# Optimization experiments

Hardware: AMD Instinct MI355X
Metric: run time of the kernel (lower is better)

The kernel has to match this reference:

```python
import jax, jax.numpy as jnp
import numpy as np
import math

EMBED_DIM = 1024
NUM_HEADS = 16
HEAD_DIM = EMBED_DIM // NUM_HEADS
ACT_BITS = 8
WGT_BITS = 8


def fake_quant(x, n_bits):
    # Per-tensor symmetric fake quantization with straight-through estimator.
    qmax = 2.0 ** (n_bits - 1) - 1.0  # 127 for 8 bits
    scale = jnp.maximum(jnp.max(jnp.abs(x)) / qmax, 1e-8)
    q = jnp.clip(jnp.round(x / scale), -qmax - 1.0, qmax) * scale
    return x + jax.lax.stop_gradient(q - x)


def setup_inputs() -> dict:
    key = jax.random.key(0)
    ks = jax.random.split(key, 7)
    S, B, D = 2048, 2, EMBED_DIM
    return {
        "query": jax.random.normal(ks[0], (S, B, D), dtype=jnp.float32),
        "key": jax.random.normal(ks[1], (S, B, D), dtype=jnp.float32),
        "value": jax.random.normal(ks[2], (S, B, D), dtype=jnp.float32),
        "Wi": jax.random.normal(ks[3], (3 * D, D), dtype=jnp.float32) * (1.0 / math.sqrt(D)),
        "bi": jax.random.normal(ks[4], (3 * D,), dtype=jnp.float32) * 0.01,
        "Wo": jax.random.normal(ks[5], (D, D), dtype=jnp.float32) * (1.0 / math.sqrt(D)),
        "bo": jax.random.normal(ks[6], (D,), dtype=jnp.float32) * 0.01,
    }


def reference(query, key, value, Wi, bi, Wo, bo):
    D, H, hd = EMBED_DIM, NUM_HEADS, HEAD_DIM
    len_q, batch, _ = query.shape
    len_k = key.shape[0]

    Wi_q = fake_quant(Wi, WGT_BITS)
    Wo_q = fake_quant(Wo, WGT_BITS)

    # in-projections (full 3D projection per input, then chunk, as in source)
    Xq = fake_quant(query @ Wi_q.T + bi, ACT_BITS)
    Xk = fake_quant(key @ Wi_q.T + bi, ACT_BITS)
    Xv = fake_quant(value @ Wi_q.T + bi, ACT_BITS)
    Q = Xq[..., :D]
    K = Xk[..., D:2 * D]
    V = Xv[..., 2 * D:]

    # [len, B, D] -> [B*H, len, hd]
    q = Q.reshape(len_q, batch * H, hd).transpose(1, 0, 2)
    k = K.reshape(len_k, batch * H, hd).transpose(1, 0, 2)
    v = V.reshape(len_k, batch * H, hd).transpose(1, 0, 2)

    q = fake_quant(q / math.sqrt(hd), ACT_BITS)
    attn = jnp.einsum('bqd,bkd->bqk', q, k)  # note: attn/softmax fake-quants in source are no-ops (result discarded)
    attn = jax.nn.softmax(attn, axis=-1)
    heads = fake_quant(jnp.einsum('bqk,bkd->bqd', attn, v), ACT_BITS)

    # [B*H, len_q, hd] -> [len_q*B, D]
    heads_reshape = heads.transpose(1, 0, 2).reshape(len_q * batch, D)
    y = (heads_reshape @ Wo_q.T + bo).reshape(len_q, batch, D)
    return fake_quant(y, ACT_BITS)
```

## Files before the change

kernel.cpp:

```cpp
#include <hip/hip_runtime.h>
#include <math.h>


typedef _Float16 f16;
typedef _Float16 half8 __attribute__((ext_vector_type(8)));
typedef _Float16 half4 __attribute__((ext_vector_type(4)));
typedef _Float16 half2v __attribute__((ext_vector_type(2)));
typedef __fp16 fp16x2 __attribute__((ext_vector_type(2)));
typedef float floatx4 __attribute__((ext_vector_type(4)));
typedef int int4v __attribute__((ext_vector_type(4)));

#define QMAX 127.0f

#define SLOT_WI 0
#define SLOT_WO 1
#define SLOT_XQ 2
#define SLOT_XK 3
#define SLOT_XV 4
#define SLOT_HD 5
#define SLOT_Y  6
#define SLOT_Q  7
#define SLOT_A  8

__device__ __forceinline__ float slot_scale(const unsigned* slots, int slot, float premul) {
  if (slot < 0) return 1.0f;
  return fmaxf(__uint_as_float(slots[slot]) * premul / QMAX, 1e-8f);
}

__device__ __forceinline__ float slot_scaleA(const unsigned* slots) {
  return fmaxf(__uint_as_float(slots[SLOT_A]) / 16256.0f, 1e-8f);
}

__device__ __forceinline__ void gl2lds16(const void* gsrc, void* ldst) {
  __builtin_amdgcn_global_load_lds((__attribute__((address_space(1))) void*)gsrc,
                                   (__attribute__((address_space(3))) void*)ldst, 16, 0, 0);
}

__device__ __forceinline__ half2v pack2(float a, float b) {
  fp16x2 r = __builtin_amdgcn_cvt_pkrtz(a, b);
  return __builtin_bit_cast(half2v, r);
}

__global__ __launch_bounds__(64) void init_slots_k(unsigned* slots) {
  if (threadIdx.x < 16) slots[threadIdx.x] = 0u;
}

__global__ __launch_bounds__(256) void absmax3_k(const float* __restrict__ Wi,
                                                 const float* __restrict__ Wo,
                                                 const float* __restrict__ q,
                                                 const float* __restrict__ k,
                                                 const float* __restrict__ v,
                                                 unsigned* __restrict__ slots) {
  __shared__ float red[256];
  int tid = threadIdx.x;
  int bid = blockIdx.x;
  const float4* x4;
  int n4, i0, stride, slot;
  if (bid < 768) {
    x4 = (const float4*)Wi; n4 = 786432; i0 = bid * 256 + tid;
    stride = 768 * 256; slot = SLOT_WI;
  } else if (bid < 1024) {
    x4 = (const float4*)Wo; n4 = 262144; i0 = (bid - 768) * 256 + tid;
    stride = 256 * 256; slot = SLOT_WO;
  } else {
    int r = bid - 1024;
    int t = r >> 9;
    x4 = (const float4*)(t == 0 ? q : (t == 1 ? k : v));
    n4 = 1048576; i0 = (r & 511) * 256 + tid;
    stride = 512 * 256; slot = SLOT_A;
  }
  float lmax = 0.f;
  for (int i = i0; i < n4; i += stride) {
    float4 vv = x4[i];
    lmax = fmaxf(lmax, fmaxf(fmaxf(fabsf(vv.x), fabsf(vv.y)), fmaxf(fabsf(vv.z), fabsf(vv.w))));
  }
  red[tid] = lmax; __syncthreads();
  for (int sh = 128; sh > 0; sh >>= 1) {
    if (tid < sh) red[tid] = fmaxf(red[tid], red[tid + sh]);
    __syncthreads();
  }
  if (tid == 0) atomicMax(&slots[slot], __float_as_uint(red[0]));
}

__global__ __launch_bounds__(256) void quantw_k(const float* __restrict__ Wi,
                                                const float* __restrict__ Wo,
                                                char* __restrict__ Wi8,
                                                char* __restrict__ Wo8,
                                                const unsigned* __restrict__ slots) {
  int tid = threadIdx.x;
  if (blockIdx.x < 768) {
    float s = slot_scale(slots, SLOT_WI, 1.0f);
    const float4* in4 = (const float4*)Wi;
    for (int i = blockIdx.x * 256 + tid; i < 786432; i += 768 * 256) {
      float4 v = in4[i];
      char4 o;
      o.x = (signed char)(int)fminf(fmaxf(rintf(v.x / s), -128.0f), 127.0f);
      o.y = (signed char)(int)fminf(fmaxf(rintf(v.y / s), -128.0f), 127.0f);
      o.z = (signed char)(int)fminf(fmaxf(rintf(v.z / s), -128.0f), 127.0f);
      o.w = (signed char)(int)fminf(fmaxf(rintf(v.w / s), -128.0f), 127.0f);
      *(char4*)(Wi8 + (size_t)i * 4) = o;
    }
  } else {
    float s = slot_scale(slots, SLOT_WO, 1.0f);
    const float4* in4 = (const float4*)Wo;
    for (int i = (blockIdx.x - 768) * 256 + tid; i < 262144; i += 256 * 256) {
      float4 v = in4[i];
      char4 o;
      o.x = (signed char)(int)fminf(fmaxf(rintf(v.x / s), -128.0f), 127.0f);
      o.y = (signed char)(int)fminf(fmaxf(rintf(v.y / s), -128.0f), 127.0f);
      o.z = (signed char)(int)fminf(fmaxf(rintf(v.z / s), -128.0f), 127.0f);
      o.w = (signed char)(int)fminf(fmaxf(rintf(v.w / s), -128.0f), 127.0f);
      *(char4*)(Wo8 + (size_t)i * 4) = o;
    }
  }
}

__global__ __launch_bounds__(256) void digitize_k(const float* __restrict__ q,
                                                  const float* __restrict__ k,
                                                  const float* __restrict__ v,
                                                  char* __restrict__ A1,
                                                  char* __restrict__ A2,
                                                  const unsigned* __restrict__ slots) {
  float inv = 1.0f / slot_scaleA(slots);
  char4* o1 = (char4*)A1;
  char4* o2 = (char4*)A2;
  for (int i = blockIdx.x * 256 + threadIdx.x; i < 3145728; i += gridDim.x * 256) {
    int t = i >> 20;
    const float4* src = (const float4*)(t == 0 ? q : (t == 1 ? k : v));
    float4 x = src[i & 1048575];
    float xs[4] = {x.x, x.y, x.z, x.w};
    signed char c1s[4], c2s[4];
#pragma unroll
    for (int u = 0; u < 4; ++u) {
      float qv = fminf(fmaxf(rintf(xs[u] * inv), -16256.0f), 16256.0f);
      float c1 = rintf(qv * 0.0078125f);
      c1s[u] = (signed char)(int)c1;
      c2s[u] = (signed char)(int)(qv - 128.0f * c1);
    }
    o1[i] = make_char4(c1s[0], c1s[1], c1s[2], c1s[3]);
    o2[i] = make_char4(c2s[0], c2s[1], c2s[2], c2s[3]);
  }
}

__global__ __launch_bounds__(256) void quantf_k(const float* __restrict__ in, float* __restrict__ out,
                                                int n4, unsigned* __restrict__ slots,
                                                int sSlot, float premul) {
  float s = slot_scale(slots, sSlot, premul);
  const float4* in4 = (const float4*)in;
  float4* out4 = (float4*)out;
  for (int i = blockIdx.x * 256 + threadIdx.x; i < n4; i += gridDim.x * 256) {
    float4 v = in4[i];
    float xs[4] = {v.x, v.y, v.z, v.w};
#pragma unroll
    for (int u = 0; u < 4; ++u) {
      float r = rintf((xs[u] * premul) / s);
      r = fminf(fmaxf(r, -128.0f), 127.0f);
      xs[u] = r * s;
    }
    out4[i] = make_float4(xs[0], xs[1], xs[2], xs[3]);
  }
}

__global__ __launch_bounds__(256) void quanti_k(const float* __restrict__ in, f16* __restrict__ out,
                                                int n4, unsigned* __restrict__ slots,
                                                int sSlot, int outAbsSlot) {
  __shared__ float red[256];
  float s = slot_scale(slots, sSlot, 1.0f);
  float lmax = 0.f;
  const float4* in4 = (const float4*)in;
  for (int i = blockIdx.x * 256 + threadIdx.x; i < n4; i += gridDim.x * 256) {
    float4 v = in4[i];
    float xs[4] = {v.x, v.y, v.z, v.w};
    half4 o;
#pragma unroll
    for (int u = 0; u < 4; ++u) {
      float r = rintf(xs[u] / s);
      r = fminf(fmaxf(r, -128.0f), 127.0f);
      o[u] = (f16)r;
      lmax = fmaxf(lmax, fabsf(r));
    }
    *(half4*)(out + (size_t)i * 4) = o;
  }
  if (outAbsSlot >= 0) {
    int tid = threadIdx.x;
    red[tid] = lmax; __syncthreads();
    for (int sh = 128; sh > 0; sh >>= 1) {
      if (tid < sh) red[tid] = fmaxf(red[tid], red[tid + sh]);
      __syncthreads();
    }
    if (tid == 0) atomicMax(&slots[outAbsSlot], __float_as_uint(red[0] * s));
  }
}

__global__ __launch_bounds__(256) void quant8_k(const float* __restrict__ in, char* __restrict__ out,
                                                int n4, const unsigned* __restrict__ slots,
                                                int sSlot) {
  float s = slot_scale(slots, sSlot, 1.0f);
  const float4* in4 = (const float4*)in;
  for (int i = blockIdx.x * 256 + threadIdx.x; i < n4; i += gridDim.x * 256) {
    float4 v = in4[i];
    char4 o;
    o.x = (signed char)(int)fminf(fmaxf(rintf(v.x / s), -128.0f), 127.0f);
    o.y = (signed char)(int)fminf(fmaxf(rintf(v.y / s), -128.0f), 127.0f);
    o.z = (signed char)(int)fminf(fmaxf(rintf(v.z / s), -128.0f), 127.0f);
    o.w = (signed char)(int)fminf(fmaxf(rintf(v.w / s), -128.0f), 127.0f);
    *(char4*)(out + (size_t)i * 4) = o;
  }
}

__global__ __launch_bounds__(256) void quantv_t_k(const float* __restrict__ Xv,
                                                  f16* __restrict__ Vt,
                                                  const unsigned* __restrict__ slots) {
  __shared__ f16 T[64][68];
  int tid = threadIdx.x;
  int bh = blockIdx.y, b = bh >> 4, h = bh & 15;
  int k0 = blockIdx.x * 64;
  float s = slot_scale(slots, SLOT_XV, 1.0f);
#pragma unroll
  for (int it = 0; it < 4; ++it) {
    int idx = tid + it * 256;
    int row = idx >> 4, dseg = idx & 15;
    float4 v = *(const float4*)(Xv + ((size_t)(k0 + row) * 2 + b) * 1024 + h * 64 + dseg * 4);
    float xs[4] = {v.x, v.y, v.z, v.w};
    half4 o;
#pragma unroll
    for (int u = 0; u < 4; ++u) {
      float r = rintf(xs[u] / s);
      o[u] = (f16)fminf(fmaxf(r, -128.0f), 127.0f);
    }
    *(half4*)&T[row][dseg * 4] = o;
  }
  __syncthreads();
#pragma unroll
  for (int it = 0; it < 2; ++it) {
    int sdx = tid + it * 256;
    int d = sdx >> 3, j8 = sdx & 7;
    half8 o;
#pragma unroll
    for (int l = 0; l < 8; ++l) {
      int pos = j8 * 8 + l;
      int tp = pos >> 5, pq = (pos & 31) >> 3, jj = pos & 7;
      int k = tp * 32 + pq * 4 + ((jj < 4) ? jj : jj + 12);
      o[l] = T[k][d];
    }
    *(half8*)(Vt + ((size_t)bh * 64 + d) * 2048 + k0 + j8 * 8) = o;
  }
}

__global__ __launch_bounds__(512, 4) void gemm_qkv_i8_k(const char* __restrict__ A1,
                                                        const char* __restrict__ A2,
                                                        const char* __restrict__ B8,
                                                        const float* __restrict__ bias,
                                                        float* __restrict__ Xout,
                                                        unsigned* __restrict__ slots) {
  __shared__ char As1[2][8192];
  __shared__ char As2[2][8192];
  __shared__ char Bs8[2][8192];
  __shared__ float red[512];

  const int K = 1024;
  int tid = threadIdx.x;
  int lane = tid & 63, w = tid >> 6;
  int wm = w >> 1, wn = w & 1;
  int quad = lane >> 4, l15 = lane & 15;
  int t = blockIdx.y >> 5;
  int m0 = (blockIdx.y & 31) * 128;
  int n0 = blockIdx.x * 128;
  size_t aoff = (size_t)t * 4194304;

  int srow = lane >> 2;
  int sgr = (lane & 3) * 16;

  const char* a1p = A1 + aoff;
  const char* a2p = A2 + aoff;

  int4v acc1[2][4], acc2[2][4];
#pragma unroll
  for (int i = 0; i < 2; ++i)
#pragma unroll
    for (int j = 0; j < 4; ++j) {
      acc1[i][j] = (int4v){0, 0, 0, 0};
      acc2[i][j] = (int4v){0, 0, 0, 0};
    }

  auto stage = [&](int buf, int kk) __attribute__((always_inline)) {
    int r0 = w * 16;
    int row = r0 + srow;
    gl2lds16(a1p + (size_t)(m0 + row) * K + kk + sgr, &As1[buf][r0 * 64]);
    gl2lds16(a2p + (size_t)(m0 + row) * K + kk + sgr, &As2[buf][r0 * 64]);
    gl2lds16(B8 + (size_t)(n0 + row) * K + kk + sgr, &Bs8[buf][r0 * 64]);
  };

  auto compute = [&](int buf) __attribute__((always_inline)) {
    int4v bf[4];
#pragma unroll
    for (int j = 0; j < 4; ++j)
      bf[j] = *(const int4v*)&Bs8[buf][(wn * 64 + j * 16 + l15) * 64 + quad * 16];
    int4v a1f[2];
#pragma unroll
    for (int i = 0; i < 2; ++i)
      a1f[i] = *(const int4v*)&As1[buf][(wm * 32 + i * 16 + l15) * 64 + quad * 16];
#pragma unroll
    for (int i = 0; i < 2; ++i)
#pragma unroll
      for (int j = 0; j < 4; ++j)
        acc1[i][j] = __builtin_amdgcn_mfma_i32_16x16x64_i8(a1f[i], bf[j], acc1[i][j], 0, 0, 0);
    int4v a2f[2];
#pragma unroll
    for (int i = 0; i < 2; ++i)
      a2f[i] = *(const int4v*)&As2[buf][(wm * 32 + i * 16 + l15) * 64 + quad * 16];
#pragma unroll
    for (int i = 0; i < 2; ++i)
#pragma unroll
      for (int j = 0; j < 4; ++j)
        acc2[i][j] = __builtin_amdgcn_mfma_i32_16x16x64_i8(a2f[i], bf[j], acc2[i][j], 0, 0, 0);
  };

  stage(0, 0);
  __syncthreads();
  for (int kt = 0; kt < 7; ++kt) {
    stage(1, (2 * kt + 1) * 64);
    compute(0);
    __syncthreads();
    stage(0, (2 * kt + 2) * 64);
    compute(1);
    __syncthreads();
  }
  stage(1, 960);
  compute(0);
  __syncthreads();
  compute(1);

  float sc = slot_scaleA(slots) * slot_scale(slots, SLOT_WI, 1.0f);
  int colLo = t * 1024;
  float* outT = Xout + aoff;
  float lmax = 0.f;
#pragma unroll
  for (int i = 0; i < 2; ++i) {
#pragma unroll
    for (int j = 0; j < 4; ++j) {
      int gn = n0 + wn * 64 + j * 16 + l15;
      float bv = bias[gn];
      bool wr = (gn >= colLo && gn < colLo + 1024);
#pragma unroll
      for (int r = 0; r < 4; ++r) {
        int gm = m0 + wm * 32 + i * 16 + quad * 4 + r;
        float vv = fmaf((float)acc1[i][j][r], 128.0f, (float)acc2[i][j][r]) * sc + bv;
        lmax = fmaxf(lmax, fabsf(vv));
        if (wr) outT[(size_t)gm * 1024 + (gn - colLo)] = vv;
      }
    }
  }
  red[tid] = lmax; __syncthreads();
  for (int sh = 256; sh > 0; sh >>= 1) {
    if (tid < sh) red[tid] = fmaxf(red[tid], red[tid + sh]);
    __syncthreads();
  }
  if (tid == 0) atomicMax(&slots[SLOT_XQ + t], __float_as_uint(red[0]));
}

__global__ __launch_bounds__(256) void gemm_i8out_k(const char* __restrict__ A8,
                                                    const char* __restrict__ B8,
                                                    const float* __restrict__ bias,
                                                    float* __restrict__ out,
                                                    unsigned* __restrict__ slots) {
  __shared__ char As8[2][8192];
  __shared__ char Bs8[2][8192];
  __shared__ float red[256];

  const int K = 1024;
  int tid = threadIdx.x;
  int lane = tid & 63, w = tid >> 6;
  int wm = w >> 1, wn = w & 1;
  int quad = lane >> 4, l15 = lane & 15;
  int m0 = blockIdx.y * 128, n0 = blockIdx.x * 128;

  int srow = lane >> 2;
  int sgr = (lane & 3) * 16;

  int4v acc[4][4];
#pragma unroll
  for (int i = 0; i < 4; ++i)
#pragma unroll
    for (int j = 0; j < 4; ++j) acc[i][j] = (int4v){0, 0, 0, 0};

  auto stage = [&](int buf, int kk) __attribute__((always_inline)) {
#pragma unroll
    for (int u = 0; u < 2; ++u) {
      int r0 = (w * 2 + u) * 16;
      int row = r0 + srow;
      gl2lds16(A8 + (size_t)(m0 + row) * K + kk + sgr, &As8[buf][r0 * 64]);
      gl2lds16(B8 + (size_t)(n0 + row) * K + kk + sgr, &Bs8[buf][r0 * 64]);
    }
  };

  auto compute = [&](int buf) __attribute__((always_inline)) {
    int4v af[4], bf[4];
#pragma unroll
    for (int i = 0; i < 4; ++i)
      af[i] = *(const int4v*)&As8[buf][(wm * 64 + i * 16 + l15) * 64 + quad * 16];
#pragma unroll
    for (int j = 0; j < 4; ++j)
      bf[j] = *(const int4v*)&Bs8[buf][(wn * 64 + j * 16 + l15) * 64 + quad * 16];
#pragma unroll
    for (int i = 0; i < 4; ++i)
#pragma unroll
      for (int j = 0; j < 4; ++j)
        acc[i][j] = __builtin_amdgcn_mfma_i32_16x16x64_i8(af[i], bf[j], acc[i][j], 0, 0, 0);
  };

  stage(0, 0);
  __syncthreads();
  for (int kt = 0; kt < 7; ++kt) {
    stage(1, (2 * kt + 1) * 64);
    compute(0);
    __syncthreads();
    stage(0, (2 * kt + 2) * 64);
    compute(1);
    __syncthreads();
  }
  stage(1, 960);
  compute(0);
  __syncthreads();
  compute(1);

  float sc = slot_scale(slots, SLOT_HD, 1.0f) * slot_scale(slots, SLOT_WO, 1.0f);
  float lmax = 0.f;
#pragma unroll
  for (int i = 0; i < 4; ++i) {
#pragma unroll
    for (int j = 0; j < 4; ++j) {
      int gn = n0 + wn * 64 + j * 16 + l15;
      float bv = bias[gn];
#pragma unroll
      for (int r = 0; r < 4; ++r) {
        int gm = m0 + wm * 64 + i * 16 + quad * 4 + r;
        float v = (float)acc[i][j][r] * sc + bv;
        lmax = fmaxf(lmax, fabsf(v));
        out[(size_t)gm * 1024 + gn] = v;
      }
    }
  }
  red[tid] = lmax; __syncthreads();
  for (int sh = 128; sh > 0; sh >>= 1) {
    if (tid < sh) red[tid] = fmaxf(red[tid], red[tid + sh]);
    __syncthreads();
  }
  if (tid == 0) atomicMax(&slots[SLOT_Y], __float_as_uint(red[0]));
}

__global__ __launch_bounds__(256) void attn_k(const f16* __restrict__ Qc,
                                              const f16* __restrict__ Kh,
                                              const f16* __restrict__ Vt,
                                              float* __restrict__ heads,
                                              unsigned* __restrict__ slots) {
  __shared__ f16 Ks[64 * 64];
  __shared__ f16 Vs[64][72];
  __shared__ float lred[4][2][16];
  __shared__ float red[256];

  int tid = threadIdx.x;
  int lane = tid & 63, w = tid >> 6;
  int quad = lane >> 4, l15 = lane & 15;
  int bh = blockIdx.y, b = bh >> 4, h = bh & 15;
  int q0 = blockIdx.x * 128;

  float s1 = slot_scale(slots, SLOT_XQ, 1.0f);
  float sq = slot_scale(slots, SLOT_Q, 0.125f);
  float sk = slot_scale(slots, SLOT_XK, 1.0f);
  float sv = slot_scale(slots, SLOT_XV, 1.0f);
  float cS = sq * sk * 1.44269504088896340736f;
  const float FOFF = 12.0f;

  half8 qf[2][2];
#pragma unroll
  for (int s = 0; s < 2; ++s) {
    const f16* qrow = Qc + ((size_t)(q0 + w * 32 + s * 16 + l15) * 2 + b) * 1024 + h * 64;
    half8 qr0 = *(const half8*)(qrow + quad * 8);
    half8 qr1 = *(const half8*)(qrow + 32 + quad * 8);
#pragma unroll
    for (int u = 0; u < 8; ++u) {
      float x0 = ((float)qr0[u] * s1) * 0.125f;
      float x1 = ((float)qr1[u] * s1) * 0.125f;
      qf[s][0][u] = (f16)fminf(fmaxf(rintf(x0 / sq), -128.0f), 127.0f);
      qf[s][1][u] = (f16)fminf(fmaxf(rintf(x1 / sq), -128.0f), 127.0f);
    }
  }

  int ksrow = lane >> 3;
  int ksp = lane & 7;
  int vr0 = tid >> 3, vs0 = (tid & 7) * 8;

  floatx4 oacc[2][4];
#pragma unroll
  for (int s = 0; s < 2; ++s)
#pragma unroll
    for (int d = 0; d < 4; ++d) oacc[s][d] = (floatx4){0.f, 0.f, 0.f, 0.f};
  float lsum[2] = {0.f, 0.f};

  const f16* vbase = Vt + (size_t)bh * 131072;

  for (int kt = 0; kt < 2048; kt += 64) {
    __syncthreads();
#pragma unroll
    for (int t = 0; t < 2; ++t) {
      int r0 = (w * 2 + t) * 8;
      int row = r0 + ksrow;
      int g = ksp ^ (row & 7);
      gl2lds16(Kh + ((size_t)(kt + row) * 2 + b) * 1024 + h * 64 + g * 8, &Ks[r0 * 64]);
    }
    half8 va = *(const half8*)(vbase + (size_t)vr0 * 2048 + kt + vs0);
    half8 vb = *(const half8*)(vbase + (size_t)(vr0 + 32) * 2048 + kt + vs0);
    *(half8*)&Vs[vr0][vs0] = va;
    *(half8*)&Vs[vr0 + 32][vs0] = vb;
    __syncthreads();

    half8 aph[2][2], apl[2][2];
#pragma unroll
    for (int t = 0; t < 4; ++t) {
      int row = t * 16 + l15;
      int g1 = quad ^ (row & 7);
      half8 kf0 = *(half8*)&Ks[row * 64 + g1 * 8];
      half8 kf1 = *(half8*)&Ks[row * 64 + (g1 ^ 4) * 8];
      int tp = t >> 1, hi = (t & 1) * 4;
#pragma unroll
      for (int s = 0; s < 2; ++s) {
        floatx4 sacc = (floatx4){0.f, 0.f, 0.f, 0.f};
        sacc = __builtin_amdgcn_mfma_f32_16x16x32_f16(kf0, qf[s][0], sacc, 0, 0, 0);
        sacc = __builtin_amdgcn_mfma_f32_16x16x32_f16(kf1, qf[s][1], sacc, 0, 0, 0);
        float p0 = __builtin_amdgcn_exp2f(fmaf(sacc[0], cS, -FOFF));
        float p1 = __builtin_amdgcn_exp2f(fmaf(sacc[1], cS, -FOFF));
        float p2 = __builtin_amdgcn_exp2f(fmaf(sacc[2], cS, -FOFF));
        float p3 = __builtin_amdgcn_exp2f(fmaf(sacc[3], cS, -FOFF));
        lsum[s] += (p0 + p1) + (p2 + p3);
        half2v h01 = pack2(p0, p1);
        half2v h23 = pack2(p2, p3);
        half2v l01 = pack2(p0 - (float)h01[0], p1 - (float)h01[1]);
        half2v l23 = pack2(p2 - (float)h23[0], p3 - (float)h23[1]);
        aph[s][tp][hi + 0] = h01[0]; aph[s][tp][hi + 1] = h01[1];
        aph[s][tp][hi + 2] = h23[0]; aph[s][tp][hi + 3] = h23[1];
        apl[s][tp][hi + 0] = l01[0]; apl[s][tp][hi + 1] = l01[1];
        apl[s][tp][hi + 2] = l23[0]; apl[s][tp][hi + 3] = l23[1];
      }
    }

#pragma unroll
    for (int d = 0; d < 4; ++d) {
      const f16* vsrow = &Vs[d * 16 + l15][0];
      half8 b0 = *(const half8*)(vsrow + quad * 8);
      half8 b1 = *(const half8*)(vsrow + 32 + quad * 8);
#pragma unroll
      for (int s = 0; s < 2; ++s) {
        oacc[s][d] = __builtin_amdgcn_mfma_f32_16x16x32_f16(aph[s][0], b0, oacc[s][d], 0, 0, 0);
        oacc[s][d] = __builtin_amdgcn_mfma_f32_16x16x32_f16(apl[s][0], b0, oacc[s][d], 0, 0, 0);
        oacc[s][d] = __builtin_amdgcn_mfma_f32_16x16x32_f16(aph[s][1], b1, oacc[s][d], 0, 0, 0);
        oacc[s][d] = __builtin_amdgcn_mfma_f32_16x16x32_f16(apl[s][1], b1, oacc[s][d], 0, 0, 0);
      }
    }
  }

#pragma unroll
  for (int s = 0; s < 2; ++s) {
    float l = lsum[s];
    l += __shfl_xor(l, 16);
    l += __shfl_xor(l, 32);
    lred[w][s][l15] = l;
  }
  float linv[2][4];
#pragma unroll
  for (int s = 0; s < 2; ++s)
#pragma unroll
    for (int r = 0; r < 4; ++r) linv[s][r] = sv / lred[w][s][quad * 4 + r];

  float lmax = 0.f;
#pragma unroll
  for (int s = 0; s < 2; ++s)
#pragma unroll
    for (int d = 0; d < 4; ++d)
#pragma unroll
      for (int r = 0; r < 4; ++r) {
        float hv = oacc[s][d][r] * linv[s][r];
        heads[((size_t)(q0 + w * 32 + s * 16 + quad * 4 + r) * 2 + b) * 1024 +
              h * 64 + d * 16 + l15] = hv;
        lmax = fmaxf(lmax, fabsf(hv));
      }
  red[tid] = lmax; __syncthreads();
  for (int sh = 128; sh > 0; sh >>= 1) {
    if (tid < sh) red[tid] = fmaxf(red[tid], red[tid + sh]);
    __syncthreads();
  }
  if (tid == 0) atomicMax(&slots[SLOT_HD], __float_as_uint(red[0]));
}

extern "C" void kernel_launch(void* const* d_in, const int* in_sizes, int n_in,
                              void* d_out, int out_size, void* d_ws, size_t ws_size,
                              hipStream_t stream) {
  (void)in_sizes; (void)n_in; (void)out_size; (void)ws_size;
  const float* query = (const float*)d_in[0];
  const float* key   = (const float*)d_in[1];
  const float* value = (const float*)d_in[2];
  const float* Wi    = (const float*)d_in[3];
  const float* bi    = (const float*)d_in[4];
  const float* Wo    = (const float*)d_in[5];
  const float* bo    = (const float*)d_in[6];
  float* out = (float*)d_out;

  char* p = (char*)d_ws;
  unsigned* slots = (unsigned*)p;            p += 1024;
  char* Wi8 = p;                             p += 3072 * 1024;
  char* Wo8 = p;                             p += 1024 * 1024;
  char* A1  = p;                             p += 12288 * 1024;
  char* A2  = p;                             p += 12288 * 1024;
  float* Hd = (float*)A1;
  f16* Kint = (f16*)(A2 + 4194304);
  float* Xq = (float*)p;                     p += 4096 * 1024 * 4;
  float* Y  = Xq;
  float* Xk = (float*)p;                     p += 4096 * 1024 * 4;
  f16* Qc   = (f16*)Xk;
  float* Xv = (float*)p;                     p += 4096 * 1024 * 4;
  char* Hint8 = (char*)Xv + 4096 * 1024 * 2;
  f16* Vt   = (f16*)p;                       p += 4096 * 1024 * 2;

  init_slots_k<<<1, 64, 0, stream>>>(slots);
  absmax3_k<<<2560, 256, 0, stream>>>(Wi, Wo, query, key, value, slots);
  quantw_k<<<1024, 256, 0, stream>>>(Wi, Wo, Wi8, Wo8, slots);
  digitize_k<<<2048, 256, 0, stream>>>(query, key, value, A1, A2, slots);

  dim3 gq(24, 96);
  gemm_qkv_i8_k<<<gq, 512, 0, stream>>>(A1, A2, Wi8, bi, Xq, slots);

  quanti_k<<<1024, 256, 0, stream>>>(Xk, Kint, 1048576, slots, SLOT_XK, -1);
  quanti_k<<<1024, 256, 0, stream>>>(Xq, Qc, 1048576, slots, SLOT_XQ, SLOT_Q);

  dim3 gvt(32, 32);
  quantv_t_k<<<gvt, 256, 0, stream>>>(Xv, Vt, slots);

  dim3 ga(16, 32);
  attn_k<<<ga, 256, 0, stream>>>(Qc, Kint, Vt, Hd, slots);

  quant8_k<<<1024, 256, 0, stream>>>(Hd, Hint8, 1048576, slots, SLOT_HD);

  dim3 g2(8, 32);
  gemm_i8out_k<<<g2, 256, 0, stream>>>(Hint8, Wo8, bo, Y, slots);

  quantf_k<<<1024, 256, 0, stream>>>(Y, out, 1048576, slots, SLOT_Y, 1.0f);
}
```

Before: 372.2 us.

## Pre-swizzle int8 GEMM operands into MFMA tile layout and widen output GEMM blocks

```diff
diff --git a/kernel.cpp b/kernel.cpp
--- a/kernel.cpp
+++ b/kernel.cpp
@@ -39,6 +39,11 @@
 __device__ __forceinline__ half2v pack2(float a, float b) {
   fp16x2 r = __builtin_amdgcn_cvt_pkrtz(a, b);
   return __builtin_bit_cast(half2v, r);
+}
+
+__device__ __forceinline__ size_t swz(int m, int k) {
+  return ((size_t)(m >> 4) << 14) + (size_t)(((k >> 6) << 10) +
+         (((k >> 4) & 3) << 8) + ((m & 15) << 4) + (k & 15));
 }
 
 __global__ __launch_bounds__(64) void init_slots_k(unsigned* slots) {
@@ -93,24 +98,26 @@
     const float4* in4 = (const float4*)Wi;
     for (int i = blockIdx.x * 256 + tid; i < 786432; i += 768 * 256) {
       float4 v = in4[i];
+      int n = i >> 8, kk = (i & 255) * 4;
       char4 o;
       o.x = (signed char)(int)fminf(fmaxf(rintf(v.x / s), -128.0f), 127.0f);
       o.y = (signed char)(int)fminf(fmaxf(rintf(v.y / s), -128.0f), 127.0f);
       o.z = (signed char)(int)fminf(fmaxf(rintf(v.z / s), -128.0f), 127.0f);
       o.w = (signed char)(int)fminf(fmaxf(rintf(v.w / s), -128.0f), 127.0f);
-      *(char4*)(Wi8 + (size_t)i * 4) = o;
+      *(char4*)(Wi8 + swz(n, kk)) = o;
     }
   } else {
     float s = slot_scale(slots, SLOT_WO, 1.0f);
     const float4* in4 = (const float4*)Wo;
     for (int i = (blockIdx.x - 768) * 256 + tid; i < 262144; i += 256 * 256) {
       float4 v = in4[i];
+      int n = i >> 8, kk = (i & 255) * 4;
       char4 o;
       o.x = (signed char)(int)fminf(fmaxf(rintf(v.x / s), -128.0f), 127.0f);
       o.y = (signed char)(int)fminf(fmaxf(rintf(v.y / s), -128.0f), 127.0f);
       o.z = (signed char)(int)fminf(fmaxf(rintf(v.z / s), -128.0f), 127.0f);
       o.w = (signed char)(int)fminf(fmaxf(rintf(v.w / s), -128.0f), 127.0f);
-      *(char4*)(Wo8 + (size_t)i * 4) = o;
+      *(char4*)(Wo8 + swz(n, kk)) = o;
     }
   }
 }
@@ -122,12 +129,12 @@
                                                   char* __restrict__ A2,
                                                   const unsigned* __restrict__ slots) {
   float inv = 1.0f / slot_scaleA(slots);
-  char4* o1 = (char4*)A1;
-  char4* o2 = (char4*)A2;
   for (int i = blockIdx.x * 256 + threadIdx.x; i < 3145728; i += gridDim.x * 256) {
     int t = i >> 20;
+    int g = i & 1048575;
     const float4* src = (const float4*)(t == 0 ? q : (t == 1 ? k : v));
-    float4 x = src[i & 1048575];
+    float4 x = src[g];
+    int m = g >> 8, kk = (g & 255) * 4;
     float xs[4] = {x.x, x.y, x.z, x.w};
     signed char c1s[4], c2s[4];
 #pragma unroll
@@ -137,8 +144,9 @@
       c1s[u] = (signed char)(int)c1;
       c2s[u] = (signed char)(int)(qv - 128.0f * c1);
     }
-    o1[i] = make_char4(c1s[0], c1s[1], c1s[2], c1s[3]);
-    o2[i] = make_char4(c2s[0], c2s[1], c2s[2], c2s[3]);
+    size_t off = (size_t)t * 4194304 + swz(m, kk);
+    *(char4*)(A1 + off) = make_char4(c1s[0], c1s[1], c1s[2], c1s[3]);
+    *(char4*)(A2 + off) = make_char4(c2s[0], c2s[1], c2s[2], c2s[3]);
   }
 }
 
@@ -199,12 +207,13 @@
   const float4* in4 = (const float4*)in;
   for (int i = blockIdx.x * 256 + threadIdx.x; i < n4; i += gridDim.x * 256) {
     float4 v = in4[i];
+    int m = i >> 8, kk = (i & 255) * 4;
     char4 o;
     o.x = (signed char)(int)fminf(fmaxf(rintf(v.x / s), -128.0f), 127.0f);
     o.y = (signed char)(int)fminf(fmaxf(rintf(v.y / s), -128.0f), 127.0f);
     o.z = (signed char)(int)fminf(fmaxf(rintf(v.z / s), -128.0f), 127.0f);
     o.w = (signed char)(int)fminf(fmaxf(rintf(v.w / s), -128.0f), 127.0f);
-    *(char4*)(out + (size_t)i * 4) = o;
+    *(char4*)(out + swz(m, kk)) = o;
   }
 }
 
@@ -247,18 +256,17 @@
   }
 }
 
-__global__ __launch_bounds__(512, 4) void gemm_qkv_i8_k(const char* __restrict__ A1,
-                                                        const char* __restrict__ A2,
-                                                        const char* __restrict__ B8,
-                                                        const float* __restrict__ bias,
-                                                        float* __restrict__ Xout,
-                                                        unsigned* __restrict__ slots) {
+__global__ __launch_bounds__(512) void gemm_qkv_i8_k(const char* __restrict__ A1,
+                                                     const char* __restrict__ A2,
+                                                     const char* __restrict__ B8,
+                                                     const float* __restrict__ bias,
+                                                     float* __restrict__ Xout,
+                                                     unsigned* __restrict__ slots) {
   __shared__ char As1[2][8192];
   __shared__ char As2[2][8192];
   __shared__ char Bs8[2][8192];
   __shared__ float red[512];
 
-  const int K = 1024;
   int tid = threadIdx.x;
   int lane = tid & 63, w = tid >> 6;
   int wm = w >> 1, wn = w & 1;
@@ -268,9 +276,6 @@
   int n0 = blockIdx.x * 128;
   size_t aoff = (size_t)t * 4194304;
 
-  int srow = lane >> 2;
-  int sgr = (lane & 3) * 16;
-
   const char* a1p = A1 + aoff;
   const char* a2p = A2 + aoff;
 
@@ -284,22 +289,22 @@
     }
 
   auto stage = [&](int buf, int kk) __attribute__((always_inline)) {
-    int r0 = w * 16;
-    int row = r0 + srow;
-    gl2lds16(a1p + (size_t)(m0 + row) * K + kk + sgr, &As1[buf][r0 * 64]);
-    gl2lds16(a2p + (size_t)(m0 + row) * K + kk + sgr, &As2[buf][r0 * 64]);
-    gl2lds16(B8 + (size_t)(n0 + row) * K + kk + sgr, &Bs8[buf][r0 * 64]);
+    size_t ac = ((size_t)((m0 >> 4) + w) << 14) + ((kk >> 6) << 10) + lane * 16;
+    size_t bc = ((size_t)((n0 >> 4) + w) << 14) + ((kk >> 6) << 10) + lane * 16;
+    gl2lds16(a1p + ac, &As1[buf][w * 1024]);
+    gl2lds16(a2p + ac, &As2[buf][w * 1024]);
+    gl2lds16(B8 + bc, &Bs8[buf][w * 1024]);
   };
 
   auto compute = [&](int buf) __attribute__((always_inline)) {
     int4v bf[4];
 #pragma unroll
     for (int j = 0; j < 4; ++j)
-      bf[j] = *(const int4v*)&Bs8[buf][(wn * 64 + j * 16 + l15) * 64 + quad * 16];
+      bf[j] = *(const int4v*)&Bs8[buf][(wn * 4 + j) * 1024 + lane * 16];
     int4v a1f[2];
 #pragma unroll
     for (int i = 0; i < 2; ++i)
-      a1f[i] = *(const int4v*)&As1[buf][(wm * 32 + i * 16 + l15) * 64 + quad * 16];
+      a1f[i] = *(const int4v*)&As1[buf][(wm * 2 + i) * 1024 + lane * 16];
 #pragma unroll
     for (int i = 0; i < 2; ++i)
 #pragma unroll
@@ -308,7 +313,7 @@
     int4v a2f[2];
 #pragma unroll
     for (int i = 0; i < 2; ++i)
-      a2f[i] = *(const int4v*)&As2[buf][(wm * 32 + i * 16 + l15) * 64 + quad * 16];
+      a2f[i] = *(const int4v*)&As2[buf][(wm * 2 + i) * 1024 + lane * 16];
 #pragma unroll
     for (int i = 0; i < 2; ++i)
 #pragma unroll
@@ -359,51 +364,45 @@
   if (tid == 0) atomicMax(&slots[SLOT_XQ + t], __float_as_uint(red[0]));
 }
 
-__global__ __launch_bounds__(256) void gemm_i8out_k(const char* __restrict__ A8,
+__global__ __launch_bounds__(512) void gemm_i8out_k(const char* __restrict__ A8,
                                                     const char* __restrict__ B8,
                                                     const float* __restrict__ bias,
                                                     float* __restrict__ out,
                                                     unsigned* __restrict__ slots) {
   __shared__ char As8[2][8192];
   __shared__ char Bs8[2][8192];
-  __shared__ float red[256];
-
-  const int K = 1024;
+  __shared__ float red[512];
+
   int tid = threadIdx.x;
   int lane = tid & 63, w = tid >> 6;
   int wm = w >> 1, wn = w & 1;
   int quad = lane >> 4, l15 = lane & 15;
   int m0 = blockIdx.y * 128, n0 = blockIdx.x * 128;
 
-  int srow = lane >> 2;
-  int sgr = (lane & 3) * 16;
-
-  int4v acc[4][4];
-#pragma unroll
-  for (int i = 0; i < 4; ++i)
+  int4v acc[2][4];
+#pragma unroll
+  for (int i = 0; i < 2; ++i)
 #pragma unroll
     for (int j = 0; j < 4; ++j) acc[i][j] = (int4v){0, 0, 0, 0};
 
   auto stage = [&](int buf, int kk) __attribute__((always_inline)) {
-#pragma unroll
-    for (int u = 0; u < 2; ++u) {
-      int r0 = (w * 2 + u) * 16;
-      int row = r0 + srow;
-      gl2lds16(A8 + (size_t)(m0 + row) * K + kk + sgr, &As8[buf][r0 * 64]);
-      gl2lds16(B8 + (size_t)(n0 + row) * K + kk + sgr, &Bs8[buf][r0 * 64]);
-    }
+    size_t ac = ((size_t)((m0 >> 4) + w) << 14) + ((kk >> 6) << 10) + lane * 16;
+    size_t bc = ((size_t)((n0 >> 4) + w) << 14) + ((kk >> 6) << 10) + lane * 16;
+    gl2lds16(A8 + ac, &As8[buf][w * 1024]);
+    gl2lds16(B8 + bc, &Bs8[buf][w * 1024]);
   };
 
   auto compute = [&](int buf) __attribute__((always_inline)) {
-    int4v af[4], bf[4];
-#pragma unroll
-    for (int i = 0; i < 4; ++i)
-      af[i] = *(const int4v*)&As8[buf][(wm * 64 + i * 16 + l15) * 64 + quad * 16];
+    int4v bf[4];
 #pragma unroll
     for (int j = 0; j < 4; ++j)
-      bf[j] = *(const int4v*)&Bs8[buf][(wn * 64 + j * 16 + l15) * 64 + quad * 16];
-#pragma unroll
-    for (int i = 0; i < 4; ++i)
+      bf[j] = *(const int4v*)&Bs8[buf][(wn * 4 + j) * 1024 + lane * 16];
+    int4v af[2];
+#pragma unroll
+    for (int i = 0; i < 2; ++i)
+      af[i] = *(const int4v*)&As8[buf][(wm * 2 + i) * 1024 + lane * 16];
+#pragma unroll
+    for (int i = 0; i < 2; ++i)
 #pragma unroll
       for (int j = 0; j < 4; ++j)
         acc[i][j] = __builtin_amdgcn_mfma_i32_16x16x64_i8(af[i], bf[j], acc[i][j], 0, 0, 0);
@@ -427,14 +426,14 @@
   float sc = slot_scale(slots, SLOT_HD, 1.0f) * slot_scale(slots, SLOT_WO, 1.0f);
   float lmax = 0.f;
 #pragma unroll
-  for (int i = 0; i < 4; ++i) {
+  for (int i = 0; i < 2; ++i) {
 #pragma unroll
     for (int j = 0; j < 4; ++j) {
       int gn = n0 + wn * 64 + j * 16 + l15;
       float bv = bias[gn];
 #pragma unroll
       for (int r = 0; r < 4; ++r) {
-        int gm = m0 + wm * 64 + i * 16 + quad * 4 + r;
+        int gm = m0 + wm * 32 + i * 16 + quad * 4 + r;
         float v = (float)acc[i][j][r] * sc + bv;
         lmax = fmaxf(lmax, fabsf(v));
         out[(size_t)gm * 1024 + gn] = v;
@@ -442,7 +441,7 @@
     }
   }
   red[tid] = lmax; __syncthreads();
-  for (int sh = 128; sh > 0; sh >>= 1) {
+  for (int sh = 256; sh > 0; sh >>= 1) {
     if (tid < sh) red[tid] = fmaxf(red[tid], red[tid + sh]);
     __syncthreads();
   }
@@ -641,7 +640,7 @@
   quant8_k<<<1024, 256, 0, stream>>>(Hd, Hint8, 1048576, slots, SLOT_HD);
 
   dim3 g2(8, 32);
-  gemm_i8out_k<<<g2, 256, 0, stream>>>(Hint8, Wo8, bo, Y, slots);
+  gemm_i8out_k<<<g2, 512, 0, stream>>>(Hint8, Wo8, bo, Y, slots);
 
   quantf_k<<<1024, 256, 0, stream>>>(Y, out, 1048576, slots, SLOT_Y, 1.0f);
 }
```

New measurement: 381.9 us. +2.6%, slower.
